# Optimization experiments

Measured on AMD Instinct MI355X. Metric: run time of the kernel, lower is better.

## Reference

```python
import jax, jax.numpy as jnp
import numpy as np

K_NN = 8        # neighbors
RADIUS = 0.1    # neighbor distance cutoff


def setup_inputs() -> dict:
    key = jax.random.key(0)
    k1, k2 = jax.random.split(key)
    B, N, KS = 2, 8192, 16  # batch, points, mask slots
    pc = jax.random.uniform(k1, (B, N, 3), dtype=jnp.float32)
    mask = jax.random.uniform(k2, (B, N, KS), dtype=jnp.float32)
    return {"pc": pc, "mask": mask}


def _knn(k, pc):
    # squared pairwise distances via gemm: (B,N,N)
    sq = jnp.sum(pc * pc, axis=-1)
    d2 = sq[:, :, None] + sq[:, None, :] - 2.0 * jnp.einsum("bnd,bmd->bnm", pc, pc)
    d2 = jnp.maximum(d2, 0.0)
    neg_d2, idx = jax.lax.top_k(-d2, k)          # k smallest distances
    dist = jnp.sqrt(jnp.maximum(-neg_d2, 0.0))   # (B,N,k) euclidean
    return dist, idx


def reference(pc, mask):
    # mask: (B,N,KS) -> (B,KS,N)
    mask_t = jnp.transpose(mask, (0, 2, 1))
    dist, idx = _knn(K_NN, pc)                   # (B,N,k) each
    # replace out-of-radius neighbors with the self index (nearest = self)
    self_idx = idx[:, :, :1]                     # (B,N,1)
    idx = jnp.where(dist > RADIUS, self_idx, idx)
    idx = jax.lax.stop_gradient(idx)
    # grouping_operation: (B,KS,N) gathered at (B,N,k) -> (B,KS,N,k)
    nn_mask = jax.vmap(lambda f, i: f[:, i])(mask_t, idx)
    # loss_norm=1: L1 norm over mask-slot dim (dim=1), mean over k, mean overall
    diff = mask_t[:, :, :, None] - nn_mask       # (B,KS,N,k)
    loss = jnp.sum(jnp.abs(diff), axis=1).mean(axis=-1)  # (B,N)
    return loss.mean()
```

## Files before the change

### kernel.cpp

```cpp
#include <hip/hip_runtime.h>

#define BATCH 2
#define NPTS  8192
#define KS    16
#define KNN   8
#define R2LOOSE 0.0101f
#define KEYMASK 0xFFFFE000u
#define NCELL   1000
#define CSTRIDE 1024

#define QB       64
#define NWAVE    8
#define NTHREADS 512
#define CAP      32
#define NBLK     (BATCH * NPTS / QB)

__device__ __forceinline__ int cell_of(float x, float y, float z) {
    int cx = (int)(x * 10.0f); cx = cx > 9 ? 9 : cx;
    int cy = (int)(y * 10.0f); cy = cy > 9 ? 9 : cy;
    int cz = (int)(z * 10.0f); cz = cz > 9 ? 9 : cz;
    return (cx * 10 + cy) * 10 + cz;
}

__global__ __launch_bounds__(1024) void build_kernel(
    const float* __restrict__ pc,
    float4* __restrict__ cs, int* __restrict__ sidx,
    int* __restrict__ cstart, float* __restrict__ out)
{
    __shared__ int h[1024];
    __shared__ int wsum[16];
    const int blk = blockIdx.x, t = threadIdx.x;
    const int b = blk >> 3, seg = blk & 7;
    const int lane = t & 63, w = t >> 6;

    h[t] = 0;
    if (blk == 0 && t == 0) out[0] = 0.0f;

    const float* p = pc + (size_t)b * NPTS * 3;
    float X[8], Y[8], Z[8]; int CC[8];
#pragma unroll
    for (int j = 0; j < 8; ++j) {
        const int i = j * 1024 + t;
        X[j] = p[3 * i]; Y[j] = p[3 * i + 1]; Z[j] = p[3 * i + 2];
        CC[j] = cell_of(X[j], Y[j], Z[j]);
    }
    __syncthreads();

    int myold = 0;
#pragma unroll
    for (int j = 0; j < 8; ++j) {
        const int old = atomicAdd(&h[CC[j]], 1);
        if (j == seg) myold = old;
        __syncthreads();
    }

    const int sum = h[t];
    int inc = sum;
#pragma unroll
    for (int off = 1; off < 64; off <<= 1) {
        const int v = __shfl_up(inc, off);
        if (lane >= off) inc += v;
    }
    if (lane == 63) wsum[w] = inc;
    __syncthreads();
    if (w == 0) {
        const int v = (lane < 16) ? wsum[lane] : 0;
        int iv = v;
#pragma unroll
        for (int off = 1; off < 16; off <<= 1) {
            const int u = __shfl_up(iv, off);
            if (lane >= off) iv += u;
        }
        if (lane < 16) wsum[lane] = iv - v;
    }
    __syncthreads();
    const int excl = inc - sum + wsum[w];
    if (seg == 0) cstart[b * CSTRIDE + t] = excl;
    __syncthreads();
    h[t] = excl;
    __syncthreads();

    float mx = X[0], my_ = Y[0], mz = Z[0]; int mc = CC[0];
#pragma unroll
    for (int j = 1; j < 8; ++j)
        if (seg == j) { mx = X[j]; my_ = Y[j]; mz = Z[j]; mc = CC[j]; }

    const int pos = h[mc] + myold;
    const float sq = fmaf(mz, mz, fmaf(my_, my_, mx * mx));
    cs[b * NPTS + pos]   = make_float4(mx, my_, mz, -0.5f * sq);
    sidx[b * NPTS + pos] = seg * 1024 + t;
}

__global__ __launch_bounds__(512) void knn_loss_kernel(
    const float4* __restrict__ cs,
    const int*    __restrict__ sidx,
    const int*    __restrict__ cstart,
    const float*  __restrict__ mask,
    float* __restrict__ out)
{
    __shared__ unsigned sbuf[CAP * NTHREADS];
    __shared__ int      fidx[QB * KNN];
    __shared__ int      qid[QB];
    __shared__ float    red[NWAVE];

    const int t = threadIdx.x;
    const int q = t & (QB - 1);
    const int s = t >> 6;
    const int su = __builtin_amdgcn_readfirstlane(s);
    const int blk = blockIdx.x;
    const int b  = blk >> 7;
    const int q0 = (blk & 127) * QB;
    const int qpos = q0 + q;

    const float4* csb = cs + b * NPTS;
    const float4 qc = csb[qpos];
    const int    qi = sidx[b * NPTS + qpos];
    if (s == 0) qid[q] = qi;

    const float qx = qc.x, qy = qc.y, qz = qc.z;
    const float qs = -2.0f * qc.w;
    const float negthr = (qs - R2LOOSE) * 0.5f;
    const unsigned SENT = (__float_as_uint(R2LOOSE) & KEYMASK) | 0x1FFFu;

    int lex = cell_of(qx, qy, qz);
    int cmn = lex, cmx = lex;
#pragma unroll
    for (int off = 32; off; off >>= 1) {
        cmn = min(cmn, __shfl_xor(cmn, off));
        cmx = max(cmx, __shfl_xor(cmx, off));
    }
    const int cfirst = __builtin_amdgcn_readfirstlane(cmn);
    const int clast  = __builtin_amdgcn_readfirstlane(cmx);

    int lo0 = cfirst - 111, h0 = clast - 89;
    int lo1 = cfirst - 11,  h1 = clast + 11;
    int lo2 = cfirst + 89,  h2 = clast + 111;
    lo0 = min(max(lo0, 0), 1000);
    lo1 = min(max(lo1, 0), 1000);
    lo2 = min(max(lo2, 0), 1000);
    int hp0 = min(max(h0 + 1, 0), 1000);
    int hp1 = min(max(h1 + 1, 0), 1000);
    int hp2 = min(max(h2 + 1, 0), 1000);
    lo1 = max(lo1, hp0);
    lo2 = max(lo2, hp1);

    const int* csp = cstart + b * CSTRIDE;
    const int P0 = __builtin_amdgcn_readfirstlane(csp[lo0]);
    const int E0 = __builtin_amdgcn_readfirstlane(csp[hp0]);
    const int P1 = __builtin_amdgcn_readfirstlane(csp[lo1]);
    const int E1 = __builtin_amdgcn_readfirstlane(csp[hp1]);
    const int P2 = __builtin_amdgcn_readfirstlane(csp[lo2]);
    const int E2 = __builtin_amdgcn_readfirstlane(csp[hp2]);
    const int L0 = max(0, E0 - P0);
    const int L1 = max(0, E1 - P1);
    const int L2 = max(0, E2 - P2);
    const int C  = L0 + L1 + L2;

    auto SPOS = [&](int g) {
        int sp = P0 + g;
        sp = (g >= L0)      ? (P1 + (g - L0))      : sp;
        sp = (g >= L0 + L1) ? (P2 + (g - L0 - L1)) : sp;
        return sp;
    };

    int cnt = 0;
    auto EVAL = [&](const float4& c, int spos) {
        const float tt = fmaf(c.x, qx, fmaf(c.y, qy, fmaf(c.z, qz, c.w)));
        const float d2 = fmaxf(fmaf(-2.0f, tt, qs), 0.0f);
        const unsigned key =
            (__float_as_uint(d2) & KEYMASK) | (unsigned)spos;
        const int slot = cnt < (CAP - 1) ? cnt : (CAP - 1);
        sbuf[slot * NTHREADS + t] = key;
        cnt += (tt >= negthr) ? 1 : 0;
    };

    {
        const int gs = (su * C) >> 3;
        const int ge = ((su + 1) * C) >> 3;
        int g = gs;
        for (; g + 8 <= ge; g += 8) {
            int sp[8]; float4 c[8];
#pragma unroll
            for (int u = 0; u < 8; ++u) sp[u] = SPOS(g + u);
#pragma unroll
            for (int u = 0; u < 8; ++u) c[u] = csb[sp[u]];
#pragma unroll
            for (int u = 0; u < 8; ++u) EVAL(c[u], sp[u]);
        }
        for (; g < ge; ++g) {
            const int sp = SPOS(g);
            const float4 c0 = csb[sp];
            EVAL(c0, sp);
        }
    }

    unsigned md[KNN];
#pragma unroll
    for (int k = 0; k < KNN; ++k) md[k] = SENT;
    const int m = cnt < CAP ? cnt : CAP;
    for (int k = 0; k < m; ++k) {
        unsigned ky = sbuf[k * NTHREADS + t];
#pragma unroll
        for (int i = 0; i < KNN; ++i) {
            const unsigned mn = min(ky, md[i]);
            const unsigned mx = max(ky, md[i]);
            md[i] = mn; ky = mx;
        }
    }
    __syncthreads();

    {
        uint4* bp = (uint4*)&sbuf[t * KNN];
        bp[0] = make_uint4(md[0], md[1], md[2], md[3]);
        bp[1] = make_uint4(md[4], md[5], md[6], md[7]);
    }
    __syncthreads();

    if (s == 0) {
        for (int l = 1; l < NWAVE; ++l) {
            const uint4* lp = (const uint4*)&sbuf[(l * QB + q) * KNN];
            const uint4 r0 = lp[0], r1 = lp[1];
            const unsigned tk[8] = {r0.x, r0.y, r0.z, r0.w,
                                    r1.x, r1.y, r1.z, r1.w};
#pragma unroll
            for (int k = 0; k < 8; ++k) {
                unsigned ky = tk[k];
                if (ky < md[KNN - 1]) {
#pragma unroll
                    for (int i = 0; i < KNN; ++i) {
                        const unsigned mn = min(ky, md[i]);
                        const unsigned mx = max(ky, md[i]);
                        md[i] = mn; ky = mx;
                    }
                }
            }
        }
#pragma unroll
        for (int k = 0; k < KNN; ++k) {
            const unsigned ky = md[k];
            int nb;
            if (ky >= SENT) {
                nb = qi;
            } else {
                const int sp = (int)(ky & 0x1FFFu);
                const float4 cc = csb[sp];
                const float dx = cc.x - qx;
                const float dy = cc.y - qy;
                const float dz = cc.z - qz;
                const float d2 = fmaf(dx, dx, fmaf(dy, dy, dz * dz));
                nb = (sqrtf(d2) > 0.1f) ? qi : sidx[b * NPTS + sp];
            }
            fidx[q * KNN + k] = nb;
        }
    }
    __syncthreads();

    const int q2 = t >> 3;
    const int j2 = t & 7;
    const int qg = qid[q2];
    const int nb = fidx[q2 * KNN + j2];
    const float* mrow = mask + ((size_t)b * NPTS + qg) * KS;
    const float* nrow = mask + ((size_t)b * NPTS + nb) * KS;
    float acc = 0.0f;
#pragma unroll
    for (int c = 0; c < KS; c += 4) {
        const float4 a = *(const float4*)(mrow + c);
        const float4 v = *(const float4*)(nrow + c);
        acc += fabsf(a.x - v.x) + fabsf(a.y - v.y) +
               fabsf(a.z - v.z) + fabsf(a.w - v.w);
    }

#pragma unroll
    for (int off = 32; off > 0; off >>= 1) acc += __shfl_down(acc, off);
    if ((t & 63) == 0) red[s] = acc;
    __syncthreads();
    if (t == 0) {
        float sum = 0.0f;
#pragma unroll
        for (int i = 0; i < NWAVE; ++i) sum += red[i];
        atomicAdd(out, sum * (1.0f / (BATCH * NPTS * KNN)));
    }
}

extern "C" void kernel_launch(void* const* d_in, const int* in_sizes, int n_in,
                              void* d_out, int out_size, void* d_ws, size_t ws_size,
                              hipStream_t stream) {
    const float* pc   = (const float*)d_in[0];
    const float* mask = (const float*)d_in[1];
    float* out = (float*)d_out;

    float4* cs     = (float4*)d_ws;
    int*    sidx   = (int*)((char*)d_ws + 262144);
    int*    cstart = (int*)((char*)d_ws + 327680);

    hipLaunchKernelGGL(build_kernel, dim3(16), dim3(1024), 0, stream,
                       pc, cs, sidx, cstart, out);
    hipLaunchKernelGGL(knn_loss_kernel, dim3(NBLK), dim3(512), 0, stream,
                       cs, sidx, cstart, mask, out);
}
```

Baseline: 82.92 us.

## Split each query across 8 lanes with LDS-staged candidate slabs and shuffle merge

Reassigns work so each query is handled by 8 lanes inside one wave instead of 8 waves. Each wave stages candidate points from 9 row-range segments into per-wave LDS slabs, and the lanes scan them strided by 8. The per-lane top-8 lists are merged with xor-shuffle bitonic merges, which replaces the shared-memory cross-wave merge and two block barriers, and each lane then resolves one neighbor. This cuts serial merge work and barriers, at the cost of extra LDS traffic, more segment bookkeeping, and a wave-local slab without a barrier that depends on lgkmcnt waits.

```diff
diff --git a/kernel.cpp b/kernel.cpp
--- a/kernel.cpp
+++ b/kernel.cpp
@@ -13,6 +13,7 @@
 #define NWAVE    8
 #define NTHREADS 512
 #define CAP      32
+#define SLAB     256
 #define NBLK     (BATCH * NPTS / QB)
 
 __device__ __forceinline__ int cell_of(float x, float y, float z) {
@@ -91,6 +92,9 @@
     sidx[b * NPTS + pos] = seg * 1024 + t;
 }
 
+#define CEX(a, b) { const unsigned mn_ = min(a, b), mx_ = max(a, b); \
+                    a = mn_; b = mx_; }
+
 __global__ __launch_bounds__(512) void knn_loss_kernel(
     const float4* __restrict__ cs,
     const int*    __restrict__ sidx,
@@ -98,24 +102,28 @@
     const float*  __restrict__ mask,
     float* __restrict__ out)
 {
+    __shared__ float4   stg4[NWAVE][SLAB];
+    __shared__ int      stgi[NWAVE][SLAB];
     __shared__ unsigned sbuf[CAP * NTHREADS];
     __shared__ int      fidx[QB * KNN];
     __shared__ int      qid[QB];
     __shared__ float    red[NWAVE];
 
     const int t = threadIdx.x;
-    const int q = t & (QB - 1);
+    const int l = t & 63;
+    const int k = l & 7;
     const int s = t >> 6;
     const int su = __builtin_amdgcn_readfirstlane(s);
+    const int Q = (t >> 3) & 63;
     const int blk = blockIdx.x;
     const int b  = blk >> 7;
     const int q0 = (blk & 127) * QB;
-    const int qpos = q0 + q;
+    const int qpos = q0 + Q;
 
     const float4* csb = cs + b * NPTS;
     const float4 qc = csb[qpos];
     const int    qi = sidx[b * NPTS + qpos];
-    if (s == 0) qid[q] = qi;
+    if (k == 0) qid[Q] = qi;
 
     const float qx = qc.x, qy = qc.y, qz = qc.z;
     const float qs = -2.0f * qc.w;
@@ -132,36 +140,22 @@
     const int cfirst = __builtin_amdgcn_readfirstlane(cmn);
     const int clast  = __builtin_amdgcn_readfirstlane(cmx);
 
-    int lo0 = cfirst - 111, h0 = clast - 89;
-    int lo1 = cfirst - 11,  h1 = clast + 11;
-    int lo2 = cfirst + 89,  h2 = clast + 111;
-    lo0 = min(max(lo0, 0), 1000);
-    lo1 = min(max(lo1, 0), 1000);
-    lo2 = min(max(lo2, 0), 1000);
-    int hp0 = min(max(h0 + 1, 0), 1000);
-    int hp1 = min(max(h1 + 1, 0), 1000);
-    int hp2 = min(max(h2 + 1, 0), 1000);
-    lo1 = max(lo1, hp0);
-    lo2 = max(lo2, hp1);
-
     const int* csp = cstart + b * CSTRIDE;
-    const int P0 = __builtin_amdgcn_readfirstlane(csp[lo0]);
-    const int E0 = __builtin_amdgcn_readfirstlane(csp[hp0]);
-    const int P1 = __builtin_amdgcn_readfirstlane(csp[lo1]);
-    const int E1 = __builtin_amdgcn_readfirstlane(csp[hp1]);
-    const int P2 = __builtin_amdgcn_readfirstlane(csp[lo2]);
-    const int E2 = __builtin_amdgcn_readfirstlane(csp[hp2]);
-    const int L0 = max(0, E0 - P0);
-    const int L1 = max(0, E1 - P1);
-    const int L2 = max(0, E2 - P2);
-    const int C  = L0 + L1 + L2;
-
-    auto SPOS = [&](int g) {
-        int sp = P0 + g;
-        sp = (g >= L0)      ? (P1 + (g - L0))      : sp;
-        sp = (g >= L0 + L1) ? (P2 + (g - L0 - L1)) : sp;
-        return sp;
-    };
+    int P[9], L[9], cum[9];
+    int run = 0, Cw = 0;
+    const int offs[9] = {-110, -100, -90, -10, 0, 10, 90, 100, 110};
+#pragma unroll
+    for (int i = 0; i < 9; ++i) {
+        int lo = cfirst + offs[i] - 1;
+        int hp = clast + offs[i] + 2;
+        lo = min(max(lo, 0), 1000);
+        hp = min(max(hp, 0), 1000);
+        lo = max(lo, run);
+        hp = max(hp, lo);
+        run = hp;
+        const int p = csp[lo], e = csp[hp];
+        P[i] = p; cum[i] = Cw; L[i] = e - p; Cw += L[i];
+    }
 
     int cnt = 0;
     auto EVAL = [&](const float4& c, int spos) {
@@ -174,32 +168,33 @@
         cnt += (tt >= negthr) ? 1 : 0;
     };
 
-    {
-        const int gs = (su * C) >> 3;
-        const int ge = ((su + 1) * C) >> 3;
-        int g = gs;
-        for (; g + 8 <= ge; g += 8) {
-            int sp[8]; float4 c[8];
-#pragma unroll
-            for (int u = 0; u < 8; ++u) sp[u] = SPOS(g + u);
-#pragma unroll
-            for (int u = 0; u < 8; ++u) c[u] = csb[sp[u]];
-#pragma unroll
-            for (int u = 0; u < 8; ++u) EVAL(c[u], sp[u]);
-        }
-        for (; g < ge; ++g) {
-            const int sp = SPOS(g);
-            const float4 c0 = csb[sp];
-            EVAL(c0, sp);
-        }
+    for (int fb = 0; fb < Cw; fb += SLAB) {
+        const int n = min(SLAB, Cw - fb);
+        for (int f = l; f < n; f += 64) {
+            const int g = fb + f;
+            int sp = P[0] + g;
+#pragma unroll
+            for (int i = 1; i < 9; ++i)
+                sp = (g >= cum[i]) ? P[i] + (g - cum[i]) : sp;
+            stg4[su][f] = csb[sp];
+            stgi[su][f] = sp;
+        }
+        asm volatile("s_waitcnt lgkmcnt(0)" ::: "memory");
+
+        for (int j = k; j < n; j += 8) {
+            const float4 c = stg4[su][j];
+            const int   sp = stgi[su][j];
+            EVAL(c, sp);
+        }
+        asm volatile("s_waitcnt lgkmcnt(0)" ::: "memory");
     }
 
     unsigned md[KNN];
 #pragma unroll
-    for (int k = 0; k < KNN; ++k) md[k] = SENT;
+    for (int kk = 0; kk < KNN; ++kk) md[kk] = SENT;
     const int m = cnt < CAP ? cnt : CAP;
-    for (int k = 0; k < m; ++k) {
-        unsigned ky = sbuf[k * NTHREADS + t];
+    for (int kk = 0; kk < m; ++kk) {
+        unsigned ky = sbuf[kk * NTHREADS + t];
 #pragma unroll
         for (int i = 0; i < KNN; ++i) {
             const unsigned mn = min(ky, md[i]);
@@ -207,51 +202,41 @@
             md[i] = mn; ky = mx;
         }
     }
-    __syncthreads();
+
+#pragma unroll
+    for (int off = 1; off <= 4; off <<= 1) {
+        unsigned bb[8], cc[8];
+#pragma unroll
+        for (int j = 0; j < 8; ++j)
+            bb[j] = (unsigned)__shfl_xor((int)md[j], off);
+#pragma unroll
+        for (int j = 0; j < 8; ++j)
+            cc[j] = min(md[j], bb[7 - j]);
+        CEX(cc[0], cc[4]); CEX(cc[1], cc[5]);
+        CEX(cc[2], cc[6]); CEX(cc[3], cc[7]);
+        CEX(cc[0], cc[2]); CEX(cc[1], cc[3]);
+        CEX(cc[4], cc[6]); CEX(cc[5], cc[7]);
+        CEX(cc[0], cc[1]); CEX(cc[2], cc[3]);
+        CEX(cc[4], cc[5]); CEX(cc[6], cc[7]);
+#pragma unroll
+        for (int j = 0; j < 8; ++j) md[j] = cc[j];
+    }
 
     {
-        uint4* bp = (uint4*)&sbuf[t * KNN];
-        bp[0] = make_uint4(md[0], md[1], md[2], md[3]);
-        bp[1] = make_uint4(md[4], md[5], md[6], md[7]);
-    }
-    __syncthreads();
-
-    if (s == 0) {
-        for (int l = 1; l < NWAVE; ++l) {
-            const uint4* lp = (const uint4*)&sbuf[(l * QB + q) * KNN];
-            const uint4 r0 = lp[0], r1 = lp[1];
-            const unsigned tk[8] = {r0.x, r0.y, r0.z, r0.w,
-                                    r1.x, r1.y, r1.z, r1.w};
-#pragma unroll
-            for (int k = 0; k < 8; ++k) {
-                unsigned ky = tk[k];
-                if (ky < md[KNN - 1]) {
-#pragma unroll
-                    for (int i = 0; i < KNN; ++i) {
-                        const unsigned mn = min(ky, md[i]);
-                        const unsigned mx = max(ky, md[i]);
-                        md[i] = mn; ky = mx;
-                    }
-                }
-            }
-        }
-#pragma unroll
-        for (int k = 0; k < KNN; ++k) {
-            const unsigned ky = md[k];
-            int nb;
-            if (ky >= SENT) {
-                nb = qi;
-            } else {
-                const int sp = (int)(ky & 0x1FFFu);
-                const float4 cc = csb[sp];
-                const float dx = cc.x - qx;
-                const float dy = cc.y - qy;
-                const float dz = cc.z - qz;
-                const float d2 = fmaf(dx, dx, fmaf(dy, dy, dz * dz));
-                nb = (sqrtf(d2) > 0.1f) ? qi : sidx[b * NPTS + sp];
-            }
-            fidx[q * KNN + k] = nb;
-        }
+        const unsigned ky = md[k];
+        int nb;
+        if (ky >= SENT) {
+            nb = qi;
+        } else {
+            const int sp = (int)(ky & 0x1FFFu);
+            const float4 cc2 = csb[sp];
+            const float dx = cc2.x - qx;
+            const float dy = cc2.y - qy;
+            const float dz = cc2.z - qz;
+            const float d2 = fmaf(dx, dx, fmaf(dy, dy, dz * dz));
+            nb = (sqrtf(d2) > 0.1f) ? qi : sidx[b * NPTS + sp];
+        }
+        fidx[Q * KNN + k] = nb;
     }
     __syncthreads();
 
```

New measurement: 71.82 us. 13.4% less time.
